# Optimization experiments

Measured on AMD Instinct MI355X. Metric: run time of the kernel, lower is better.

Reference implementation:

```python
import jax, jax.numpy as jnp
import numpy as np

EOS = 130


def setup_inputs() -> dict:
    key = jax.random.key(0)
    ks = jax.random.split(key, 16)
    B, H, W, C = 32, 12, 32, 512   # encoder feature map
    V, E, D = 600, 256, 512        # vocab, embed_dim, decoder_hidden
    T = 192
    s = lambda *d: 1.0 / np.sqrt(d[-1])
    inp = {
        "encoder_outputs": jax.random.normal(ks[0], (B, H, W, C), jnp.float32),
        "tgt_tokens": jax.random.randint(ks[1], (B, T), 0, V, jnp.int64),
        # embedding table (padding_idx=0 row zeroed)
        "emb_table": (jax.random.normal(ks[2], (V, E), jnp.float32) * 0.02).at[0].set(0.0),
        # LSTMCell params, gate order i,f,g,o; stored (in, 4D) / (4D,)
        "W_ih": jax.random.normal(ks[3], (E + D, 4 * D), jnp.float32) * s(E + D),
        "b_ih": jnp.zeros((4 * D,), jnp.float32),
        "W_hh": jax.random.normal(ks[4], (D, 4 * D), jnp.float32) * s(D),
        "b_hh": jnp.zeros((4 * D,), jnp.float32),
        # attention
        "W_h": jax.random.normal(ks[5], (D, D), jnp.float32) * s(D),
        "W_v": jax.random.normal(ks[6], (C, D), jnp.float32) * s(C),
        "v": jax.random.normal(ks[7], (D, 1), jnp.float32) * s(D),
        # output path
        "W_c": jax.random.normal(ks[8], (D + C, D), jnp.float32) * s(D + C),
        "b_c": jnp.zeros((D,), jnp.float32),
        "W_out": jax.random.normal(ks[9], (D, V), jnp.float32) * s(D),
        "b_out": jnp.zeros((V,), jnp.float32),
    }
    return inp


def _decode(encoder_outputs, tgt_tokens, emb_table, W_ih, b_ih, W_hh, b_hh,
            W_h, W_v, v, W_c, b_c, W_out, b_out):
    B, H, W_, C = encoder_outputs.shape
    D = W_h.shape[0]
    enc = encoder_outputs.reshape(B, H * W_, C)          # (B, N, C)
    Wv = enc @ W_v                                       # (B, N, D) precompute (step-invariant)

    def step(carry, tok_t):
        hx, cx, o_prev, input_token, finished = carry
        emb = emb_table[input_token]                     # (B, E)
        rnn_in = jnp.concatenate([emb, o_prev], axis=-1)
        gates = rnn_in @ W_ih + b_ih + hx @ W_hh + b_hh  # (B, 4D)
        i, f, g, o = jnp.split(gates, 4, axis=-1)
        cx = jax.nn.sigmoid(f) * cx + jax.nn.sigmoid(i) * jnp.tanh(g)
        hx = jax.nn.sigmoid(o) * jnp.tanh(cx)
        # Bahdanau attention
        score = jnp.squeeze(jnp.tanh(hx[:, None, :] @ W_h + Wv) @ v, -1)  # (B, N)
        alpha = jax.nn.softmax(score, axis=1)
        context = jnp.einsum('bn,bnc->bc', alpha, enc)
        o_t = jnp.tanh(jnp.concatenate([hx, context], axis=-1) @ W_c + b_c)
        logits_t = o_t @ W_out + b_out                   # (B, V)
        next_token = tok_t                               # teacher forcing (ratio=1.0)
        finished = finished | (next_token == EOS)
        input_token = jnp.where(finished, 0, next_token)
        return (hx, cx, o_t, input_token, finished), (logits_t, alpha)

    hx = jnp.zeros((B, D), encoder_outputs.dtype)
    cx = jnp.zeros_like(hx)
    o0 = jnp.zeros_like(hx)
    tok0 = jnp.zeros((B,), tgt_tokens.dtype)             # sos_index = 0
    fin0 = jnp.zeros((B,), bool)
    xs = tgt_tokens[:, 1:].T                             # (T-1, B)
    _, (logits, alphas) = jax.lax.scan(step, (hx, cx, o0, tok0, fin0), xs)
    return logits.transpose(1, 0, 2), alphas.transpose(1, 0, 2)  # (B,T-1,V), (B,T-1,N)


def reference(encoder_outputs, tgt_tokens, emb_table, W_ih, b_ih, W_hh, b_hh,
              W_h, W_v, v, W_c, b_c, W_out, b_out):
    return _decode(encoder_outputs, tgt_tokens, emb_table, W_ih, b_ih, W_hh, b_hh,
                   W_h, W_v, v, W_c, b_c, W_out, b_out)
```

## Files before the change

### kernel.cpp

```cpp
#include <hip/hip_runtime.h>
#include <cstdint>

#define Bb 32
#define Cc 512
#define Nn 384
#define Vv 600
#define Ee 256
#define Dd 512
#define Tt 192
#define Ss 191
#define EOS_TOK 130
#define BD (Bb*Dd)
#define NBLK 256
#define NTHR 512

#define OFF_TOK   0
#define OFF_SHIFT 8192
#define OFF_WV    8256
#define OFF_HXT   6299712
#define OFF_XO    6332480
#define OFF_HXB   6348864
#define OFF_DEN   6365248
#define OFF_Q     6373440
#define OFF_CTXB  6389824
#define OFF_OBUF  6406208
#define OFF_BAR   9551936

#define LOGITS_SZ (Bb*Ss*Vv)
#define ALPHA_SZ  (Bb*Ss*Nn)

__device__ __forceinline__ float sigm_(float x) {
    float e = __expf(-x);
    return __builtin_amdgcn_rcpf(1.0f + e);
}
__device__ __forceinline__ float tanh_(float x) {
    float xc = fminf(15.0f, fmaxf(-15.0f, x));
    float e = __expf(2.0f * xc);
    return (e - 1.0f) * __builtin_amdgcn_rcpf(e + 1.0f);
}

__device__ __forceinline__ void st_dev(float* p, float v) {
    __hip_atomic_store(p, v, __ATOMIC_RELAXED, __HIP_MEMORY_SCOPE_AGENT);
}
__device__ __forceinline__ float ld1_dev(const float* p) {
    return __hip_atomic_load(p, __ATOMIC_RELAXED, __HIP_MEMORY_SCOPE_AGENT);
}
__device__ __forceinline__ float2 ld2_dev(const float* p) {
    unsigned long long u = __hip_atomic_load((const unsigned long long*)p,
                                             __ATOMIC_RELAXED,
                                             __HIP_MEMORY_SCOPE_AGENT);
    float2 f;
    f.x = __uint_as_float((unsigned int)u);
    f.y = __uint_as_float((unsigned int)(u >> 32));
    return f;
}

__device__ __forceinline__ void w_arrive(int* flags, int ibar) {
    __syncthreads();
    if (threadIdx.x == 0)
        __hip_atomic_store(&flags[blockIdx.x * 16], ibar + 1, __ATOMIC_RELAXED,
                           __HIP_MEMORY_SCOPE_AGENT);
}
__device__ __forceinline__ void w_wait(int* flags, int* genv, int ibar) {
    const int target = ibar + 1;
    if (blockIdx.x == 0) {
        if (threadIdx.x < 64) {
            int l = threadIdx.x * 4;
            for (;;) {
                int f0 = __hip_atomic_load(&flags[(l + 0) * 16], __ATOMIC_RELAXED,
                                           __HIP_MEMORY_SCOPE_AGENT);
                int f1 = __hip_atomic_load(&flags[(l + 1) * 16], __ATOMIC_RELAXED,
                                           __HIP_MEMORY_SCOPE_AGENT);
                int f2 = __hip_atomic_load(&flags[(l + 2) * 16], __ATOMIC_RELAXED,
                                           __HIP_MEMORY_SCOPE_AGENT);
                int f3 = __hip_atomic_load(&flags[(l + 3) * 16], __ATOMIC_RELAXED,
                                           __HIP_MEMORY_SCOPE_AGENT);
                if (__all(f0 >= target && f1 >= target &&
                          f2 >= target && f3 >= target)) break;
                __builtin_amdgcn_s_sleep(1);
            }
            if (threadIdx.x < 32)
                __hip_atomic_store(&genv[threadIdx.x * 16], target,
                                   __ATOMIC_RELAXED, __HIP_MEMORY_SCOPE_AGENT);
        }
    } else if (threadIdx.x == 0) {
        int* g = &genv[(blockIdx.x >> 3) * 16];
        while (__hip_atomic_load(g, __ATOMIC_RELAXED,
                                 __HIP_MEMORY_SCOPE_AGENT) < target)
            __builtin_amdgcn_s_sleep(2);
    }
    __syncthreads();
}

__device__ __forceinline__ void poll8(int* base, int grp, int target) {
    if (threadIdx.x < 64) {
        int* g = &base[(grp * 8 + (threadIdx.x & 7)) * 16];
        while (__hip_atomic_load(g, __ATOMIC_RELAXED,
                                 __HIP_MEMORY_SCOPE_AGENT) < target)
            __builtin_amdgcn_s_sleep(1);
    }
    __syncthreads();
}

__global__ void k_setup(const int* __restrict__ tgt, const float* __restrict__ vv,
                        float* zbase, int* bar, int* tok, float* shiftbuf) {
    int gid = blockIdx.x * 256 + threadIdx.x;
    for (int i = gid; i < 73728; i += 96 * 256) zbase[i] = 0.f;
    if (gid < 16896) bar[gid] = 0;
    if (blockIdx.x == 0) {
        __shared__ int is64;
        if (threadIdx.x == 0) {
            int a = 1;
            for (int k = 0; k < 32; ++k) if (tgt[2 * k + 1] != 0) a = 0;
            is64 = a;
        }
        __syncthreads();
        int b = threadIdx.x;
        if (b < Bb) {
            int fin = 0;
            tok[0 * Bb + b] = 0;
            for (int s = 1; s < Ss; ++s) {
                int li = b * Tt + s;
                int nt = is64 ? tgt[2 * li] : tgt[li];
                if (nt == EOS_TOK) fin = 1;
                tok[s * Bb + b] = fin ? 0 : nt;
            }
        }
    }
    if (blockIdx.x == 1) {
        __shared__ float sred[256];
        int tid = threadIdx.x;
        sred[tid] = fabsf(vv[tid]) + fabsf(vv[tid + 256]);
        __syncthreads();
        for (int s = 128; s > 0; s >>= 1) {
            if (tid < s) sred[tid] += sred[tid + s];
            __syncthreads();
        }
        if (tid == 0) shiftbuf[0] = sred[0];
    }
}

__global__ void k_embx(const float* __restrict__ emb, const int* __restrict__ tok,
                       float* __restrict__ obuf) {
    int i = blockIdx.x * 256 + threadIdx.x;
    if (i < Ss * 8192) {
        int t = i >> 13, e = i & 8191;
        int k = e >> 5, b = e & 31;
        obuf[(size_t)(t + 1) * BD + e] = emb[(size_t)tok[t * 32 + b] * Ee + k];
    }
}

__global__ void k_wv(const float* __restrict__ enc, const float* __restrict__ Wv_w,
                     float* __restrict__ Wv) {
    int b = blockIdx.x / 24, nt = blockIdx.x % 24, n0 = nt * 16;
    __shared__ float encL[16 * 512];
    for (int i = 0; i < 32; ++i) {
        int e = threadIdx.x + i * 256;
        int ni = e >> 9, c = e & 511;
        encL[e] = enc[((b * Nn) + (n0 + ni)) * Cc + c];
    }
    __syncthreads();
    int d0 = threadIdx.x, d1 = threadIdx.x + 256;
    float a0[16], a1[16];
#pragma unroll
    for (int i = 0; i < 16; ++i) { a0[i] = 0.f; a1[i] = 0.f; }
    for (int c = 0; c < 512; ++c) {
        float w0 = Wv_w[c * Dd + d0], w1 = Wv_w[c * Dd + d1];
#pragma unroll
        for (int i = 0; i < 16; ++i) {
            float ev = encL[i * 512 + c];
            a0[i] += ev * w0; a1[i] += ev * w1;
        }
    }
#pragma unroll
    for (int i = 0; i < 16; ++i) {
        Wv[((b * Nn) + (n0 + i)) * Dd + d0] = a0[i];
        Wv[((b * Nn) + (n0 + i)) * Dd + d1] = a1[i];
    }
}

__global__ __launch_bounds__(NTHR) void k_decode(
    const float* __restrict__ enc, const float* __restrict__ W_ih,
    const float* __restrict__ b_ih, const float* __restrict__ W_hh,
    const float* __restrict__ b_hh, const float* __restrict__ W_h,
    const float* __restrict__ vv, const float* __restrict__ W_c,
    const float* __restrict__ b_c, const float* __restrict__ Wv,
    const float* __restrict__ shiftbuf,
    float* __restrict__ hxT, float* __restrict__ xo, float* __restrict__ hxB,
    float* __restrict__ den, float* __restrict__ q, float* __restrict__ ctxB,
    float* __restrict__ obuf, float* __restrict__ alpha_e, int* bar)
{
    __shared__ float Wg[1280 * 8];
    __shared__ float scratch[8192];
    __shared__ float cxL[64];

    int* flags  = bar;
    int* genv   = bar + 4096;
    int* qdone  = bar + 4608;
    int* dedone = bar + 8704;
    int* adone  = bar + 12800;

    const int tid = threadIdx.x, bid = blockIdx.x;
    const int lane = tid & 63;
    const int d0 = bid * 2;
    const int bp = tid & 15;
    const int ab = bid >> 3;
    const int n0 = (bid & 7) * 48;
    const int cg = bid & 7;
    const int w  = tid >> 6;

    for (int k = tid; k < 1280; k += NTHR) {
        const float* src = (k < 768) ? (W_ih + (size_t)k * 2048)
                                     : (W_hh + (size_t)(k - 768) * 2048);
#pragma unroll
        for (int g = 0; g < 4; ++g) {
            Wg[k * 8 + g * 2 + 0] = src[g * 512 + d0 + 0];
            Wg[k * 8 + g * 2 + 1] = src[g * 512 + d0 + 1];
        }
    }
    if (tid < 64) cxL[tid] = 0.f;
    float v8[8];
#pragma unroll
    for (int i = 0; i < 8; ++i) v8[i] = vv[lane * 8 + i];
    float4 wva[6], wvb[6];
#pragma unroll
    for (int r = 0; r < 6; ++r) {
        const float* wv = Wv + ((size_t)(ab * Nn + n0 + w * 6 + r)) * 512 + lane * 8;
        wva[r] = *(const float4*)wv;
        wvb[r] = *(const float4*)(wv + 4);
    }
    float encR[48];
#pragma unroll
    for (int i = 0; i < 48; ++i)
        encR[i] = enc[((size_t)(ab * Nn + n0 + i)) * 512 + tid];
    const float SHIFT = shiftbuf[0];
    const float bcF = b_c[cg * 64 + (tid & 63)];
    float bsum0 = 0.f, bsum1 = 0.f, bsum2 = 0.f, bsum3 = 0.f;
    if (tid < 64) {
        int dd = tid >> 5;
        int d = d0 + dd;
        bsum0 = b_ih[0 * 512 + d] + b_hh[0 * 512 + d];
        bsum1 = b_ih[1 * 512 + d] + b_hh[1 * 512 + d];
        bsum2 = b_ih[2 * 512 + d] + b_hh[2 * 512 + d];
        bsum3 = b_ih[3 * 512 + d] + b_hh[3 * 512 + d];
    }
    __syncthreads();

    for (int t = 0; t < Ss; ++t) {
        const int rd = t & 1, wr = 1 - rd;
        const float* hxT_rd = hxT + rd * 16384;
        float*       hxT_wr = hxT + wr * 16384;

        {
            const float* embx_t = obuf + (size_t)(t + 1) * BD;
            const float* xo2 = xo - 256 * 32;
            const float* hx2 = hxT_rd - 768 * 32;
            int ks = tid >> 4;
            int k0 = ks * 40;
            float ax[8], ay[8];
#pragma unroll
            for (int i = 0; i < 8; ++i) { ax[i] = 0.f; ay[i] = 0.f; }
            if (t) {
#pragma unroll
                for (int kb = 0; kb < 5; ++kb) {
                    int kbase = k0 + kb * 8;
                    if (kbase >= 256 && kbase < 768) continue;
                    const float* base = (kbase < 256) ? embx_t : hx2;
                    float2 xv[8];
#pragma unroll
                    for (int j = 0; j < 8; ++j)
                        xv[j] = ld2_dev(base + (kbase + j) * 32 + 2 * bp);
#pragma unroll
                    for (int j = 0; j < 8; ++j) {
                        int k = kbase + j;
                        float4 wA = *(const float4*)&Wg[k * 8];
                        float4 wB = *(const float4*)&Wg[k * 8 + 4];
                        ax[0] += xv[j].x * wA.x; ay[0] += xv[j].y * wA.x;
                        ax[1] += xv[j].x * wA.y; ay[1] += xv[j].y * wA.y;
                        ax[2] += xv[j].x * wA.z; ay[2] += xv[j].y * wA.z;
                        ax[3] += xv[j].x * wA.w; ay[3] += xv[j].y * wA.w;
                        ax[4] += xv[j].x * wB.x; ay[4] += xv[j].y * wB.x;
                        ax[5] += xv[j].x * wB.y; ay[5] += xv[j].y * wB.y;
                        ax[6] += xv[j].x * wB.z; ay[6] += xv[j].y * wB.z;
                        ax[7] += xv[j].x * wB.w; ay[7] += xv[j].y * wB.w;
                    }
                }
                w_wait(flags, genv, t - 1);
                if (tid < 64)
                    st_dev(&ctxB[bid * 64 + tid], 0.f);
#pragma unroll
                for (int kb = 0; kb < 5; ++kb) {
                    int kbase = k0 + kb * 8;
                    if (kbase < 256 || kbase >= 768) continue;
                    float2 xv[8];
#pragma unroll
                    for (int j = 0; j < 8; ++j)
                        xv[j] = ld2_dev(xo2 + (kbase + j) * 32 + 2 * bp);
#pragma unroll
                    for (int j = 0; j < 8; ++j) {
                        int k = kbase + j;
                        float4 wA = *(const float4*)&Wg[k * 8];
                        float4 wB = *(const float4*)&Wg[k * 8 + 4];
                        ax[0] += xv[j].x * wA.x; ay[0] += xv[j].y * wA.x;
                        ax[1] += xv[j].x * wA.y; ay[1] += xv[j].y * wA.y;
                        ax[2] += xv[j].x * wA.z; ay[2] += xv[j].y * wA.z;
                        ax[3] += xv[j].x * wA.w; ay[3] += xv[j].y * wA.w;
                        ax[4] += xv[j].x * wB.x; ay[4] += xv[j].y * wB.x;
                        ax[5] += xv[j].x * wB.y; ay[5] += xv[j].y * wB.y;
                        ax[6] += xv[j].x * wB.z; ay[6] += xv[j].y * wB.z;
                        ax[7] += xv[j].x * wB.w; ay[7] += xv[j].y * wB.w;
                    }
                }
            } else {
                if (tid < 64)
                    st_dev(&ctxB[bid * 64 + tid], 0.f);
            }
#pragma unroll
            for (int c = 0; c < 8; ++c) {
                scratch[(ks * 8 + c) * 32 + 2 * bp]     = ax[c];
                scratch[(ks * 8 + c) * 32 + 2 * bp + 1] = ay[c];
            }
            __syncthreads();
            if (tid < 256) {
                int col = tid >> 5, b2 = tid & 31;
                float s = 0.f;
#pragma unroll
                for (int k2 = 0; k2 < 32; ++k2) s += scratch[(k2 * 8 + col) * 32 + b2];
                scratch[col * 32 + b2] = s;
            }
            __syncthreads();
            if (tid < 64) {
                int dd = tid >> 5, b2 = tid & 31;
                float gi = scratch[(0 * 2 + dd) * 32 + b2] + bsum0;
                float gf = scratch[(1 * 2 + dd) * 32 + b2] + bsum1;
                float gg = scratch[(2 * 2 + dd) * 32 + b2] + bsum2;
                float go = scratch[(3 * 2 + dd) * 32 + b2] + bsum3;
                float c = sigm_(gf) * cxL[tid] + sigm_(gi) * tanh_(gg);
                cxL[tid] = c;
                float h = sigm_(go) * tanh_(c);
                st_dev(&hxT_wr[(d0 + dd) * 32 + b2], h);
                st_dev(&hxB[b2 * 512 + d0 + dd], h);
            }
        }
        __syncthreads();
        if (tid == 0)
            __hip_atomic_store(&adone[bid * 16], t + 1, __ATOMIC_RELAXED,
                               __HIP_MEMORY_SCOPE_AGENT);

        {
            float* hxL  = scratch;
            float* gred = scratch + 512;
            int col = tid & 63, kseg = tid >> 6;
            {
                int* g = &adone[(kseg * 32 + (tid & 31)) * 16];
                while (__hip_atomic_load(g, __ATOMIC_RELAXED,
                                         __HIP_MEMORY_SCOPE_AGENT) < t + 1)
                    __builtin_amdgcn_s_sleep(1);
            }
            hxL[kseg * 64 + col] = ld1_dev(&hxB[ab * 512 + kseg * 64 + col]);
            const float* wp = W_h + (size_t)(kseg * 64) * 512 + cg * 64 + col;
            const float* xr = hxL + kseg * 64;
            float a = 0.f;
#pragma unroll 8
            for (int kk = 0; kk < 64; ++kk)
                a += wp[(size_t)kk * 512] * xr[kk];
            gred[kseg * 72 + col] = a;
            __syncthreads();
            if (tid < 64) {
                float s = 0.f;
#pragma unroll
                for (int k2 = 0; k2 < 8; ++k2) s += gred[k2 * 72 + tid];
                st_dev(&q[ab * 512 + cg * 64 + tid], s);
            }
            __syncthreads();
            if (tid == 0)
                __hip_atomic_store(&qdone[bid * 16], t + 1, __ATOMIC_RELAXED,
                                   __HIP_MEMORY_SCOPE_AGENT);
        }

        {
            poll8(qdone, ab, t + 1);
            float* esc = scratch;
            float q8[8];
#pragma unroll
            for (int j = 0; j < 4; ++j) {
                float2 qv = ld2_dev(&q[ab * 512 + lane * 8 + 2 * j]);
                q8[2 * j] = qv.x; q8[2 * j + 1] = qv.y;
            }
#pragma unroll
            for (int r = 0; r < 6; ++r) {
                float s = v8[0] * tanh_(q8[0] + wva[r].x) + v8[1] * tanh_(q8[1] + wva[r].y)
                        + v8[2] * tanh_(q8[2] + wva[r].z) + v8[3] * tanh_(q8[3] + wva[r].w)
                        + v8[4] * tanh_(q8[4] + wvb[r].x) + v8[5] * tanh_(q8[5] + wvb[r].y)
                        + v8[6] * tanh_(q8[6] + wvb[r].z) + v8[7] * tanh_(q8[7] + wvb[r].w);
#pragma unroll
                for (int off = 32; off > 0; off >>= 1)
                    s += __shfl_down(s, off, 64);
                if (lane == 0) esc[w * 6 + r] = __expf(s - SHIFT);
            }
            __syncthreads();
            if (tid < 48)
                alpha_e[((size_t)ab * Ss + t) * Nn + n0 + tid] = esc[tid];
            if (tid == 0) {
                float sd = 0.f;
                for (int i = 0; i < 48; ++i) sd += esc[i];
                atomicAdd(&den[t * 32 + ab], sd);
            }
            float acc = 0.f;
#pragma unroll 8
            for (int i = 0; i < 48; ++i)
                acc += esc[i] * encR[i];
            atomicAdd(&ctxB[ab * 512 + tid], acc);
            __syncthreads();
            if (tid == 0)
                __hip_atomic_store(&dedone[bid * 16], t + 1, __ATOMIC_RELAXED,
                                   __HIP_MEMORY_SCOPE_AGENT);
        }

        {
            float* xF   = scratch;
            float* gred = scratch + 1024;
            int col = tid & 63, kseg = tid >> 6;
            if (kseg < 4) {
                xF[kseg * 128 + col]      = ld1_dev(&hxB[ab * 512 + kseg * 128 + col]);
                xF[kseg * 128 + 64 + col] = ld1_dev(&hxB[ab * 512 + kseg * 128 + 64 + col]);
            } else {
                int* g = &dedone[(ab * 8 + (tid & 7)) * 16];
                while (__hip_atomic_load(g, __ATOMIC_RELAXED,
                                         __HIP_MEMORY_SCOPE_AGENT) < t + 1)
                    __builtin_amdgcn_s_sleep(1);
                float rdn = 1.0f / ld1_dev(&den[t * 32 + ab]);
                int base = (kseg - 4) * 128;
                xF[512 + base + col]      = ld1_dev(&ctxB[ab * 512 + base + col]) * rdn;
                xF[512 + base + 64 + col] = ld1_dev(&ctxB[ab * 512 + base + 64 + col]) * rdn;
            }
            const float* wp = W_c + (size_t)(kseg * 128) * 512 + cg * 64 + col;
            const float* xr = xF + kseg * 128;
            float a = 0.f;
#pragma unroll 8
            for (int kk = 0; kk < 128; ++kk)
                a += wp[(size_t)kk * 512] * xr[kk];
            gred[kseg * 72 + col] = a;
            __syncthreads();
            if (tid < 64) {
                float s = bcF;
#pragma unroll
                for (int k2 = 0; k2 < 8; ++k2) s += gred[k2 * 72 + tid];
                float o = tanh_(s);
                st_dev(&xo[(cg * 64 + tid) * 32 + ab], o);
                obuf[(size_t)(t + 1) * BD + ab * 512 + cg * 64 + tid] = o;
            }
        }
        w_arrive(flags, t);
    }
}

__global__ void k_logits(const float* __restrict__ obuf, const float* __restrict__ W_out,
                         const float* __restrict__ b_out, float* __restrict__ out_logits) {
    int b = blockIdx.x / 24, tt = blockIdx.x % 24;
    int t0 = tt * 8;
    int tmax = min(8, Ss - t0);
    __shared__ float oL[8 * 512];
    int tid = threadIdx.x;
    for (int i = 0; i < 16; ++i) {
        int e = tid + i * 256;
        int ti = e >> 9, d = e & 511;
        oL[e] = (ti < tmax) ? obuf[(size_t)(t0 + ti + 1) * BD + b * Dd + d] : 0.f;
    }
    __syncthreads();
    int v0 = tid, v1 = tid + 256, v2 = tid + 512;
    bool h2 = (v2 < Vv);
    int v2c = h2 ? v2 : 0;
    float acc[3][8];
#pragma unroll
    for (int s = 0; s < 3; ++s)
#pragma unroll
        for (int ti = 0; ti < 8; ++ti) acc[s][ti] = 0.f;
    for (int d = 0; d < 512; ++d) {
        float w0 = W_out[d * Vv + v0];
        float w1 = W_out[d * Vv + v1];
        float w2 = W_out[d * Vv + v2c];
#pragma unroll
        for (int ti = 0; ti < 8; ++ti) {
            float o = oL[ti * 512 + d];
            acc[0][ti] += o * w0; acc[1][ti] += o * w1; acc[2][ti] += o * w2;
        }
    }
    for (int ti = 0; ti < tmax; ++ti) {
        size_t base = (size_t)b * (Ss * Vv) + (size_t)(t0 + ti) * Vv;
        out_logits[base + v0] = acc[0][ti] + b_out[v0];
        out_logits[base + v1] = acc[1][ti] + b_out[v1];
        if (h2) out_logits[base + v2] = acc[2][ti] + b_out[v2];
    }
}

__global__ void k_anorm(float* __restrict__ alph, const float* __restrict__ den) {
    int i = blockIdx.x * 256 + threadIdx.x;
    if (i < ALPHA_SZ) {
        int bt = i / Nn;
        int t = bt % Ss, b = bt / Ss;
        alph[i] = alph[i] / den[t * 32 + b];
    }
}

extern "C" void kernel_launch(void* const* d_in, const int* in_sizes, int n_in,
                              void* d_out, int out_size, void* d_ws, size_t ws_size,
                              hipStream_t stream) {
    const float* enc   = (const float*)d_in[0];
    const int*   tgt   = (const int*)d_in[1];
    const float* emb   = (const float*)d_in[2];
    const float* W_ih  = (const float*)d_in[3];
    const float* b_ih  = (const float*)d_in[4];
    const float* W_hh  = (const float*)d_in[5];
    const float* b_hh  = (const float*)d_in[6];
    const float* W_h   = (const float*)d_in[7];
    const float* W_v   = (const float*)d_in[8];
    const float* vv    = (const float*)d_in[9];
    const float* W_c   = (const float*)d_in[10];
    const float* b_c   = (const float*)d_in[11];
    const float* W_out = (const float*)d_in[12];
    const float* b_out = (const float*)d_in[13];

    float* wsf   = (float*)d_ws;
    int*   tok   = (int*)d_ws;
    float* shiftb= wsf + OFF_SHIFT;
    float* Wv    = wsf + OFF_WV;
    float* hxT   = wsf + OFF_HXT;
    float* xo    = wsf + OFF_XO;
    float* hxB   = wsf + OFF_HXB;
    float* den   = wsf + OFF_DEN;
    float* q     = wsf + OFF_Q;
    float* ctxB  = wsf + OFF_CTXB;
    float* obuf  = wsf + OFF_OBUF;
    int*   bar   = (int*)(wsf + OFF_BAR);

    float* out_logits = (float*)d_out;
    float* out_alphas = (float*)d_out + LOGITS_SZ;

    k_setup<<<96, 256, 0, stream>>>(tgt, vv, hxT, bar, tok, shiftb);
    k_embx<<<(Ss * 8192 + 255) / 256, 256, 0, stream>>>(emb, tok, obuf);
    k_wv<<<768, 256, 0, stream>>>(enc, W_v, Wv);
    k_decode<<<NBLK, NTHR, 0, stream>>>(enc, W_ih, b_ih, W_hh, b_hh, W_h, vv,
                                        W_c, b_c, Wv, shiftb,
                                        hxT, xo, hxB, den, q, ctxB, obuf,
                                        out_alphas, bar);
    k_logits<<<768, 256, 0, stream>>>(obuf, W_out, b_out, out_logits);
    k_anorm<<<(ALPHA_SZ + 255) / 256, 256, 0, stream>>>(out_alphas, den);
}
```

Before: 5.629 ms.

## Move global barrier to after LSTM step and use targeted flags for output dependencies

Moves the grid-wide barrier from the end of each timestep to just after the LSTM cell update, and double-buffers hxB so the next step's writes do not race with readers. The previous wait on all blocks before the LSTM gate accumulation is replaced by polling only the 40 output-stage flags that block depends on, via a new per-block fdone flag. The attention stage now reads hx without per-producer polling, relying on the barrier. This reshapes the synchronisation graph to shorten the critical path, but adds more scratch memory and fine-grained flag traffic.

Result: no change. 5.582 ms (-0.9%).

```diff
diff --git a/kernel.cpp b/kernel.cpp
--- a/kernel.cpp
+++ b/kernel.cpp
@@ -20,11 +20,11 @@
 #define OFF_HXT   6299712
 #define OFF_XO    6332480
 #define OFF_HXB   6348864
-#define OFF_DEN   6365248
-#define OFF_Q     6373440
-#define OFF_CTXB  6389824
-#define OFF_OBUF  6406208
-#define OFF_BAR   9551936
+#define OFF_DEN   6381632
+#define OFF_Q     6389824
+#define OFF_CTXB  6406208
+#define OFF_OBUF  6422592
+#define OFF_BAR   9568320
 
 #define LOGITS_SZ (Bb*Ss*Vv)
 #define ALPHA_SZ  (Bb*Ss*Nn)
@@ -55,14 +55,12 @@
     return f;
 }
 
-__device__ __forceinline__ void w_arrive(int* flags, int ibar) {
+__device__ __forceinline__ void gbar(int* flags, int* genv, int ibar) {
     __syncthreads();
+    const int target = ibar + 1;
     if (threadIdx.x == 0)
-        __hip_atomic_store(&flags[blockIdx.x * 16], ibar + 1, __ATOMIC_RELAXED,
+        __hip_atomic_store(&flags[blockIdx.x * 16], target, __ATOMIC_RELAXED,
                            __HIP_MEMORY_SCOPE_AGENT);
-}
-__device__ __forceinline__ void w_wait(int* flags, int* genv, int ibar) {
-    const int target = ibar + 1;
     if (blockIdx.x == 0) {
         if (threadIdx.x < 64) {
             int l = threadIdx.x * 4;
@@ -105,7 +103,7 @@
 __global__ void k_setup(const int* __restrict__ tgt, const float* __restrict__ vv,
                         float* zbase, int* bar, int* tok, float* shiftbuf) {
     int gid = blockIdx.x * 256 + threadIdx.x;
-    for (int i = gid; i < 73728; i += 96 * 256) zbase[i] = 0.f;
+    for (int i = gid; i < 90112; i += 96 * 256) zbase[i] = 0.f;
     if (gid < 16896) bar[gid] = 0;
     if (blockIdx.x == 0) {
         __shared__ int is64;
@@ -198,7 +196,7 @@
     int* genv   = bar + 4096;
     int* qdone  = bar + 4608;
     int* dedone = bar + 8704;
-    int* adone  = bar + 12800;
+    int* fdone  = bar + 12800;
 
     const int tid = threadIdx.x, bid = blockIdx.x;
     const int lane = tid & 63;
@@ -207,6 +205,7 @@
     const int ab = bid >> 3;
     const int n0 = (bid & 7) * 48;
     const int cg = bid & 7;
+    const int cgA = bid >> 5;
     const int w  = tid >> 6;
 
     for (int k = tid; k < 1280; k += NTHR) {
@@ -250,6 +249,7 @@
         const int rd = t & 1, wr = 1 - rd;
         const float* hxT_rd = hxT + rd * 16384;
         float*       hxT_wr = hxT + wr * 16384;
+        float*       hxB_t  = hxB + (t & 1) * 16384;
 
         {
             const float* embx_t = obuf + (size_t)(t + 1) * BD;
@@ -285,7 +285,15 @@
                         ax[7] += xv[j].x * wB.w; ay[7] += xv[j].y * wB.w;
                     }
                 }
-                w_wait(flags, genv, t - 1);
+                if (tid < 40) {
+                    int fl = (tid < 32) ? (tid * 8 + cgA)
+                                        : ((bid >> 3) * 8 + (tid - 32));
+                    int* g = &fdone[fl * 16];
+                    while (__hip_atomic_load(g, __ATOMIC_RELAXED,
+                                             __HIP_MEMORY_SCOPE_AGENT) < t)
+                        __builtin_amdgcn_s_sleep(1);
+                }
+                __syncthreads();
                 if (tid < 64)
                     st_dev(&ctxB[bid * 64 + tid], 0.f);
 #pragma unroll
@@ -339,25 +347,17 @@
                 cxL[tid] = c;
                 float h = sigm_(go) * tanh_(c);
                 st_dev(&hxT_wr[(d0 + dd) * 32 + b2], h);
-                st_dev(&hxB[b2 * 512 + d0 + dd], h);
-            }
-        }
-        __syncthreads();
-        if (tid == 0)
-            __hip_atomic_store(&adone[bid * 16], t + 1, __ATOMIC_RELAXED,
-                               __HIP_MEMORY_SCOPE_AGENT);
+                st_dev(&hxB_t[b2 * 512 + d0 + dd], h);
+            }
+        }
+        gbar(flags, genv, t);
 
         {
             float* hxL  = scratch;
             float* gred = scratch + 512;
+            hxL[tid] = ld1_dev(&hxB_t[ab * 512 + tid]);
+            __syncthreads();
             int col = tid & 63, kseg = tid >> 6;
-            {
-                int* g = &adone[(kseg * 32 + (tid & 31)) * 16];
-                while (__hip_atomic_load(g, __ATOMIC_RELAXED,
-                                         __HIP_MEMORY_SCOPE_AGENT) < t + 1)
-                    __builtin_amdgcn_s_sleep(1);
-            }
-            hxL[kseg * 64 + col] = ld1_dev(&hxB[ab * 512 + kseg * 64 + col]);
             const float* wp = W_h + (size_t)(kseg * 64) * 512 + cg * 64 + col;
             const float* xr = hxL + kseg * 64;
             float a = 0.f;
@@ -418,22 +418,14 @@
         }
 
         {
+            poll8(dedone, ab, t + 1);
             float* xF   = scratch;
             float* gred = scratch + 1024;
+            float rdn = 1.0f / ld1_dev(&den[t * 32 + ab]);
+            xF[tid]       = ld1_dev(&hxB_t[ab * 512 + tid]);
+            xF[512 + tid] = ld1_dev(&ctxB[ab * 512 + tid]) * rdn;
+            __syncthreads();
             int col = tid & 63, kseg = tid >> 6;
-            if (kseg < 4) {
-                xF[kseg * 128 + col]      = ld1_dev(&hxB[ab * 512 + kseg * 128 + col]);
-                xF[kseg * 128 + 64 + col] = ld1_dev(&hxB[ab * 512 + kseg * 128 + 64 + col]);
-            } else {
-                int* g = &dedone[(ab * 8 + (tid & 7)) * 16];
-                while (__hip_atomic_load(g, __ATOMIC_RELAXED,
-                                         __HIP_MEMORY_SCOPE_AGENT) < t + 1)
-                    __builtin_amdgcn_s_sleep(1);
-                float rdn = 1.0f / ld1_dev(&den[t * 32 + ab]);
-                int base = (kseg - 4) * 128;
-                xF[512 + base + col]      = ld1_dev(&ctxB[ab * 512 + base + col]) * rdn;
-                xF[512 + base + 64 + col] = ld1_dev(&ctxB[ab * 512 + base + 64 + col]) * rdn;
-            }
             const float* wp = W_c + (size_t)(kseg * 128) * 512 + cg * 64 + col;
             const float* xr = xF + kseg * 128;
             float a = 0.f;
@@ -450,8 +442,11 @@
                 st_dev(&xo[(cg * 64 + tid) * 32 + ab], o);
                 obuf[(size_t)(t + 1) * BD + ab * 512 + cg * 64 + tid] = o;
             }
-        }
-        w_arrive(flags, t);
+            __syncthreads();
+            if (tid == 0)
+                __hip_atomic_store(&fdone[bid * 16], t + 1, __ATOMIC_RELAXED,
+                                   __HIP_MEMORY_SCOPE_AGENT);
+        }
     }
 }
 
```
